# Kernel optimization log

Hardware: AMD Instinct MI355X
Metric: run time of the kernel (lower is better)

The kernel has to match this reference:

```python
import jax, jax.numpy as jnp
import numpy as np

B, T, E = 16, 1024, 1024
G, N, D = 4, 8, 128
V = 2048


def setup_inputs() -> dict:
    key = jax.random.key(0)
    k1, k2, k3, k4 = jax.random.split(key, 4)
    x_emb = jax.random.normal(k1, (B, T, E), dtype=jnp.float32)
    W_in = jax.random.normal(k2, (E, G * N * D), dtype=jnp.float32) / np.sqrt(E)
    R = jax.random.normal(k3, (G, N, D, D), dtype=jnp.float32) / np.sqrt(D)
    b = jnp.zeros((G, N, D), dtype=jnp.float32)
    W_proj = jax.random.normal(k4, (V, N * D), dtype=jnp.float32) / np.sqrt(D)
    b_proj = jnp.zeros((V,), dtype=jnp.float32)
    return {"x_emb": x_emb, "W_in": W_in, "R": R, "b": b, "W_proj": W_proj, "b_proj": b_proj}


def reference(x_emb, W_in, R, b, W_proj, b_proj):
    # Input projection for all timesteps at once: [B,T,G,N,D]
    Bx, Tx, Ex = x_emb.shape
    Wx = jnp.einsum('bte,eg->btg', x_emb, W_in).reshape(Bx, Tx, G, N, D)

    def step(carry, wx_t):
        h, c = carry  # [B,N,D] each
        # per-head matrix recurrence: R[g] @ h  -> [B,G,N,D]
        gates = wx_t + jnp.einsum('gnde,bne->bgnd', R, h) + b
        i = jax.nn.sigmoid(gates[:, 0])
        f = jax.nn.sigmoid(gates[:, 1])
        z = jnp.tanh(gates[:, 2])
        o = jax.nn.sigmoid(gates[:, 3])
        c_new = f * c + i * z
        h_new = o * jnp.tanh(c_new)
        return (h_new, c_new), h_new

    h0 = jnp.zeros((Bx, N, D), dtype=x_emb.dtype)
    c0 = jnp.zeros((Bx, N, D), dtype=x_emb.dtype)
    (hN, cN), hs = jax.lax.scan(step, (h0, c0), jnp.swapaxes(Wx, 0, 1))  # hs: [T,B,N,D]
    h_flat = jnp.swapaxes(hs, 0, 1).reshape(Bx, Tx, N * D)
    logits = jnp.einsum('btn,vn->btv', h_flat, W_proj) + b_proj
    return logits
```

## Files before the change

### kernel.cpp

```cpp
#include <hip/hip_runtime.h>
#include <hip/hip_bf16.h>

#define DEV __device__ __forceinline__

using bf16 = __hip_bfloat16;
typedef __attribute__((ext_vector_type(8))) short short8v;
typedef __attribute__((ext_vector_type(4))) float f32x4;

constexpr int Bq = 16, Tq = 1024, Eq = 1024, Gq = 4, Nq = 8, Dq = 128, Vq = 2048;
constexpr int M1 = Bq * Tq;
constexpr int N1q = Gq * Nq * Dq;
constexpr int K1 = Eq;
constexpr int K2 = Nq * Dq;
constexpr int N2 = Vq;

DEV unsigned short bfu(float x) {
  union { bf16 h; unsigned short u; } cv;
  cv.h = __float2bfloat16(x);
  return cv.u;
}

DEV float rcp_(float x) { return __builtin_amdgcn_rcpf(x); }
DEV float sigm(float x) { return rcp_(1.0f + __expf(-x)); }
DEV float tanh_(float x) { return fmaf(2.0f, rcp_(1.0f + __expf(-2.0f * x)), -1.0f); }

#define GLD16(gp, lp)                                                       \
  __builtin_amdgcn_global_load_lds(                                        \
      (const __attribute__((address_space(1))) void*)(gp),                 \
      (__attribute__((address_space(3))) void*)(lp), 16, 0, 0)

__global__ __launch_bounds__(256) void cast_f32_bf16(const float* __restrict__ s,
                                                     bf16* __restrict__ d, int n4) {
  const int i = blockIdx.x * 256 + threadIdx.x;
  if (i >= n4) return;
  const float4 v = ((const float4*)s)[i];
  ushort4 u;
  u.x = bfu(v.x); u.y = bfu(v.y); u.z = bfu(v.z); u.w = bfu(v.w);
  ((ushort4*)d)[i] = u;
}

__global__ __launch_bounds__(256) void transpose_cast_perm(const float* __restrict__ s,
                                                           bf16* __restrict__ d,
                                                           int SK, int SN) {
  __shared__ float t[32][33];
  const int n0 = blockIdx.x * 32, k0 = blockIdx.y * 32;
  const int tx = threadIdx.x & 31, ty = threadIdx.x >> 5;
#pragma unroll
  for (int i = 0; i < 32; i += 8)
    t[ty + i][tx] = s[(size_t)(k0 + ty + i) * SN + n0 + tx];
  __syncthreads();
#pragma unroll
  for (int i = 0; i < 32; i += 8) {
    const int c = n0 + ty + i;
    const int g = c >> 10, n = (c >> 7) & 7, dd = c & 127;
    const int rp = n * 512 + dd * 4 + g;
    d[(size_t)rp * SK + k0 + tx] = __float2bfloat16(t[tx][ty + i]);
  }
}

__global__ __launch_bounds__(256) void zero_flags(unsigned int* __restrict__ f) {
  f[blockIdx.x * 256 + threadIdx.x] = 0u;
}

__global__ __launch_bounds__(256) void gemm_out(const bf16* __restrict__ A,
                                                const bf16* __restrict__ Bt,
                                                float* __restrict__ C,
                                                const float* __restrict__ bp,
                                                int K, int N) {
  __shared__ bf16 As[128 * 32];
  __shared__ bf16 Bs[128 * 32];
  const int m0 = blockIdx.y * 128, n0 = blockIdx.x * 128;
  const int tid = threadIdx.x;
  const int lane = tid & 63, w = tid >> 6;
  const int wm = w >> 1, wn = w & 1;

  const int srow = lane >> 2, scol = (lane & 3) * 8;
  const int ca = w * 2;
  const bf16* Ag0 = A + (size_t)(m0 + ca * 16 + srow) * K + scol;
  const bf16* Ag1 = Ag0 + (size_t)16 * K;
  const bf16* Bg0 = Bt + (size_t)(n0 + ca * 16 + srow) * K + scol;
  const bf16* Bg1 = Bg0 + (size_t)16 * K;
  bf16* Al0 = As + ca * 512;
  bf16* Al1 = Al0 + 512;
  bf16* Bl0 = Bs + ca * 512;
  bf16* Bl1 = Bl0 + 512;

  f32x4 acc[4][4] = {};
  const int rr = lane & 15;
  const int kb = (lane >> 4) * 8;

  for (int k0 = 0; k0 < K; k0 += 32) {
    GLD16(Ag0 + k0, Al0);
    GLD16(Ag1 + k0, Al1);
    GLD16(Bg0 + k0, Bl0);
    GLD16(Bg1 + k0, Bl1);
    __syncthreads();
    short8v af[4], bfr[4];
#pragma unroll
    for (int i = 0; i < 4; ++i) {
      af[i]  = *(const short8v*)&As[(wm * 64 + i * 16 + rr) * 32 + kb];
      bfr[i] = *(const short8v*)&Bs[(wn * 64 + i * 16 + rr) * 32 + kb];
    }
#pragma unroll
    for (int i = 0; i < 4; ++i)
#pragma unroll
      for (int j = 0; j < 4; ++j)
        acc[i][j] = __builtin_amdgcn_mfma_f32_16x16x32_bf16(af[i], bfr[j], acc[i][j], 0, 0, 0);
    __syncthreads();
  }

  const int crow = (lane >> 4) * 4, ccol = lane & 15;
  float bv[4];
#pragma unroll
  for (int j = 0; j < 4; ++j) bv[j] = bp[n0 + wn * 64 + j * 16 + ccol];
#pragma unroll
  for (int i = 0; i < 4; ++i)
#pragma unroll
    for (int j = 0; j < 4; ++j) {
      const size_t base =
          (size_t)(m0 + wm * 64 + i * 16 + crow) * N + (n0 + wn * 64 + j * 16 + ccol);
#pragma unroll
      for (int jj = 0; jj < 4; ++jj)
        C[base + (size_t)jj * N] = acc[i][j][jj] + bv[j];
    }
}

__global__ __launch_bounds__(512) void fused_xw_lstm(
    const bf16* __restrict__ xb, const bf16* __restrict__ WiT,
    bf16* __restrict__ Wx, const float* __restrict__ bp,
    const float* __restrict__ R, bf16* __restrict__ h_all,
    unsigned int* flags) {
  __shared__ bf16 As[2][128 * 32];
  __shared__ bf16 Bs[2][128 * 32];
  __shared__ __align__(16) unsigned short hl[2][4][144];

  const int bid = blockIdx.x;
  const int tid = threadIdx.x;

  if (bid < 224) {
    const int lane = tid & 63;
    const int w8 = tid >> 6;
    const int ts = w8 >> 2;
    const int w = w8 & 3;
    const int wm = w >> 1, wn = w & 1;
    const int srow = lane >> 2, scol = (lane & 3) * 8;
    const int rr = lane & 15, kb = (lane >> 4) * 8;
    const int crow = (lane >> 4) * 4, ccol = lane & 15;
    bf16* Al0 = &As[ts][w * 1024];
    bf16* Al1 = Al0 + 512;
    bf16* Bl0 = &Bs[ts][w * 1024];
    bf16* Bl1 = Bl0 + 512;

    for (int pi = bid; pi < 2048; pi += 224) {
      const int tix = pi * 2 + ts;
      const int s = tix >> 9;
      const int rem = tix & 511;
      const int bn = rem >> 2, q = rem & 3;
      const int b = bn >> 3, n = bn & 7;
      const int m0 = (b * 8 + s) * 128;
      const int n0 = (n * 4 + q) * 128;

      const bf16* Ag0 = xb + (size_t)(m0 + w * 32 + srow) * 1024 + scol;
      const bf16* Ag1 = Ag0 + (size_t)16 * 1024;
      const bf16* Bg0 = WiT + (size_t)(n0 + w * 32 + srow) * 1024 + scol;
      const bf16* Bg1 = Bg0 + (size_t)16 * 1024;

      f32x4 acc[4][4] = {};
      for (int k0 = 0; k0 < 1024; k0 += 32) {
        GLD16(Ag0 + k0, Al0);
        GLD16(Ag1 + k0, Al1);
        GLD16(Bg0 + k0, Bl0);
        GLD16(Bg1 + k0, Bl1);
        __syncthreads();
        short8v af[4], bfr[4];
#pragma unroll
        for (int i = 0; i < 4; ++i) {
          af[i]  = *(const short8v*)&As[ts][(wm * 64 + i * 16 + rr) * 32 + kb];
          bfr[i] = *(const short8v*)&Bs[ts][(wn * 64 + i * 16 + rr) * 32 + kb];
        }
#pragma unroll
        for (int i = 0; i < 4; ++i)
#pragma unroll
          for (int j = 0; j < 4; ++j)
            acc[i][j] = __builtin_amdgcn_mfma_f32_16x16x32_bf16(af[i], bfr[j], acc[i][j], 0, 0, 0);
        __syncthreads();
      }

      {
        bf16* C = Wx;
#pragma unroll
        for (int i = 0; i < 4; ++i)
#pragma unroll
          for (int j = 0; j < 4; ++j) {
            const int pc = n0 + wn * 64 + j * 16 + ccol;
            const int nn = pc >> 9, gd = pc & 511;
            const int g = gd & 3, dd = gd >> 2;
            const float bvj = bp[(g * 8 + nn) * 128 + dd];
#pragma unroll
            for (int jj = 0; jj < 4; ++jj) {
              const int row = m0 + wm * 64 + i * 16 + crow + jj;
              const int bb = row >> 10, t = row & 1023;
              const size_t idx = (((size_t)(bb * 8 + nn) << 10) + t) * 512 + gd;
              C[idx] = __float2bfloat16(acc[i][j][jj] + bvj);
            }
          }
      }
      __syncthreads();
      if (tid == 0) {
        __threadfence();
#pragma unroll
        for (int k = 0; k < 2; ++k) {
          const int tx2 = pi * 2 + k;
          const int s2 = tx2 >> 9, bn2 = (tx2 & 511) >> 2;
          __hip_atomic_fetch_add(&flags[bn2 * 8 + s2], 1u,
                                 __ATOMIC_RELEASE, __HIP_MEMORY_SCOPE_AGENT);
        }
      }
    }
  } else {
    const int cid = bid - 224;
    const int n = cid & 7, bq = cid >> 3;
    const int w = tid >> 6, lane = tid & 63;
    const int lg = lane >> 4, lc = lane & 15;
    const int bloc = lc & 3;
    const int ci = lc >> 2;
    const int dsite = 16 * w + 4 * ci + lg;

    short8v Af[4][4];
#pragma unroll
    for (int tau = 0; tau < 4; ++tau) {
      const int gd = 64 * w + 16 * tau + lc;
      const int g = gd & 3, d = gd >> 2;
      const float* rbase = R + ((size_t)(g * 8 + n) * 128 + d) * 128;
#pragma unroll
      for (int kf = 0; kf < 4; ++kf) {
        const float* rp = rbase + 32 * kf + 8 * lg;
        const float4 r0 = *(const float4*)rp;
        const float4 r1 = *(const float4*)(rp + 4);
        short8v bv;
        bv[0] = (short)bfu(r0.x); bv[1] = (short)bfu(r0.y);
        bv[2] = (short)bfu(r0.z); bv[3] = (short)bfu(r0.w);
        bv[4] = (short)bfu(r1.x); bv[5] = (short)bfu(r1.y);
        bv[6] = (short)bfu(r1.z); bv[7] = (short)bfu(r1.w);
        Af[tau][kf] = bv;
      }
    }

    for (int i = tid; i < 4 * 144; i += 512) (&hl[0][0][0])[i] = 0;
    __syncthreads();

    const bf16* wxb =
        Wx + ((size_t)((bq * 4 + bloc) * 8 + n) << 10) * 512 + dsite * 4;
    bf16* hout = h_all + ((size_t)(bq * 4 + bloc) << 20) + n * 128 + dsite;

    float c = 0.f;

    for (int s = 0; s < 8; ++s) {
      if (tid == 0) {
#pragma unroll
        for (int j = 0; j < 4; ++j) {
          const int fidx = ((bq * 4 + j) * 8 + n) * 8 + s;
          while (__hip_atomic_load(&flags[fidx], __ATOMIC_RELAXED,
                                   __HIP_MEMORY_SCOPE_AGENT) < 4u)
            __builtin_amdgcn_s_sleep(2);
        }
        __threadfence();
      }
      __syncthreads();

      ushort4 wxr[4];
#pragma unroll
      for (int u = 0; u < 4; ++u)
        wxr[u] = *(const ushort4*)(wxb + (size_t)(s * 128 + u) * 512);

      const int tend = s * 128 + 128;
      for (int t0 = s * 128; t0 < tend; t0 += 4) {
#pragma unroll
        for (int u = 0; u < 4; ++u) {
          const int t = t0 + u;
          const unsigned short* hb = &hl[t & 1][0][0];
          short8v Bf[4];
#pragma unroll
          for (int kf = 0; kf < 4; ++kf)
            Bf[kf] = *(const short8v*)(hb + bloc * 144 + kf * 32 + lg * 8);

          const ushort4 wxc = wxr[u];

          f32x4 acc[4];
#pragma unroll
          for (int tau = 0; tau < 4; ++tau) {
            acc[tau][0] = 0.f; acc[tau][1] = 0.f;
            acc[tau][2] = 0.f; acc[tau][3] = 0.f;
          }
#pragma unroll
          for (int kf = 0; kf < 4; ++kf)
#pragma unroll
            for (int tau = 0; tau < 4; ++tau)
              acc[tau] = __builtin_amdgcn_mfma_f32_16x16x32_bf16(
                  Af[tau][kf], Bf[kf], acc[tau], 0, 0, 0);

          {
            const int tp = (t + 4 < tend) ? (t + 4) : (tend - 1);
            wxr[u] = *(const ushort4*)(wxb + (size_t)tp * 512);
          }

          float pre0 = (ci & 2) ? ((ci & 1) ? acc[3][0] : acc[2][0])
                                : ((ci & 1) ? acc[1][0] : acc[0][0]);
          float pre1 = (ci & 2) ? ((ci & 1) ? acc[3][1] : acc[2][1])
                                : ((ci & 1) ? acc[1][1] : acc[0][1]);
          float pre2 = (ci & 2) ? ((ci & 1) ? acc[3][2] : acc[2][2])
                                : ((ci & 1) ? acc[1][2] : acc[0][2]);
          float pre3 = (ci & 2) ? ((ci & 1) ? acc[3][3] : acc[2][3])
                                : ((ci & 1) ? acc[1][3] : acc[0][3]);
          pre0 += __uint_as_float((unsigned)wxc.x << 16);
          pre1 += __uint_as_float((unsigned)wxc.y << 16);
          pre2 += __uint_as_float((unsigned)wxc.z << 16);
          pre3 += __uint_as_float((unsigned)wxc.w << 16);

          const float i_ = sigm(pre0);
          const float f_ = sigm(pre1);
          const float z_ = tanh_(pre2);
          const float o_ = sigm(pre3);
          c = f_ * c + i_ * z_;
          const float h = o_ * tanh_(c);
          const bf16 h16 = __float2bfloat16(h);

          hl[(t + 1) & 1][bloc][dsite] = ((const unsigned short*)&h16)[0];
          hout[(size_t)t << 10] = h16;

          __builtin_amdgcn_sched_barrier(0);
          asm volatile("s_waitcnt lgkmcnt(0)" ::: "memory");
          __builtin_amdgcn_sched_barrier(0);
          __builtin_amdgcn_s_barrier();
          __builtin_amdgcn_sched_barrier(0);
        }
      }
    }
  }
}

extern "C" void kernel_launch(void* const* d_in, const int* in_sizes, int n_in,
                              void* d_out, int out_size, void* d_ws, size_t ws_size,
                              hipStream_t stream) {
  const float* x_emb = (const float*)d_in[0];
  const float* W_in  = (const float*)d_in[1];
  const float* R     = (const float*)d_in[2];
  const float* bias  = (const float*)d_in[3];
  const float* W_prj = (const float*)d_in[4];
  const float* b_prj = (const float*)d_in[5];

  char* ws = (char*)d_ws;
  bf16* xb  = (bf16*)ws;
  bf16* WiT = (bf16*)(ws + (size_t)M1 * K1 * 2);
  bf16* Wpb = WiT + (size_t)N1q * K1;
  bf16* H   = Wpb + (size_t)N2 * K2;
  unsigned int* flags = (unsigned int*)(ws + ((size_t)76 << 20));
  bf16* Wx = (bf16*)d_out;

  cast_f32_bf16<<<(M1 * K1 / 4 + 255) / 256, 256, 0, stream>>>(x_emb, xb, M1 * K1 / 4);
  transpose_cast_perm<<<dim3(N1q / 32, K1 / 32), 256, 0, stream>>>(W_in, WiT, K1, N1q);
  cast_f32_bf16<<<(N2 * K2 / 4 + 255) / 256, 256, 0, stream>>>(W_prj, Wpb, N2 * K2 / 4);
  zero_flags<<<4, 256, 0, stream>>>(flags);

  fused_xw_lstm<<<dim3(256), dim3(512), 0, stream>>>(xb, WiT, Wx, bias, R, H, flags);

  gemm_out<<<dim3(N2 / 128, M1 / 128), 256, 0, stream>>>(
      H, Wpb, (float*)d_out, b_prj, K2, N2);
}
```

Baseline: 805.7 us.

## Share A tile across wave groups and pipeline GEMM loads with 4-stage LDS ring

The input-projection GEMM blocks now load the A (x) tile once and share it between the two wave groups, each of which computes a different 128-column N tile. Previously each group loaded its own A and B tiles. The K loop becomes a 4-buffer ring that prefetches two chunks ahead, using explicit vmcnt waits and raw s_barrier instead of two __syncthreads per iteration. The aim is to halve A traffic and hide global-to-LDS latency, at the cost of more LDS for the recurrent blocks sharing the kernel and tighter hand-written waitcnt logic. The flag update is also merged into a single atomic add of 2.

```diff
diff --git a/kernel.cpp b/kernel.cpp
--- a/kernel.cpp
+++ b/kernel.cpp
@@ -28,6 +28,13 @@
   __builtin_amdgcn_global_load_lds(                                        \
       (const __attribute__((address_space(1))) void*)(gp),                 \
       (__attribute__((address_space(3))) void*)(lp), 16, 0, 0)
+
+#define SBAR0() __builtin_amdgcn_sched_barrier(0)
+#define RAWBAR()                                                            \
+  do { SBAR0(); __builtin_amdgcn_s_barrier(); SBAR0(); } while (0)
+#define VMW6() asm volatile("s_waitcnt vmcnt(6)" ::: "memory")
+#define VMW3() asm volatile("s_waitcnt vmcnt(3)" ::: "memory")
+#define VMW0() asm volatile("s_waitcnt vmcnt(0)" ::: "memory")
 
 __global__ __launch_bounds__(256) void cast_f32_bf16(const float* __restrict__ s,
                                                      bf16* __restrict__ d, int n4) {
@@ -130,8 +137,8 @@
     bf16* __restrict__ Wx, const float* __restrict__ bp,
     const float* __restrict__ R, bf16* __restrict__ h_all,
     unsigned int* flags) {
-  __shared__ bf16 As[2][128 * 32];
-  __shared__ bf16 Bs[2][128 * 32];
+  __shared__ bf16 Ab[4][128 * 32];
+  __shared__ bf16 Bb[4][2][128 * 32];
   __shared__ __align__(16) unsigned short hl[2][4][144];
 
   const int bid = blockIdx.x;
@@ -141,58 +148,76 @@
     const int lane = tid & 63;
     const int w8 = tid >> 6;
     const int ts = w8 >> 2;
-    const int w = w8 & 3;
-    const int wm = w >> 1, wn = w & 1;
-    const int srow = lane >> 2, scol = (lane & 3) * 8;
+    const int w4 = w8 & 3;
+    const int wm = w4 >> 1, wn = w4 & 1;
     const int rr = lane & 15, kb = (lane >> 4) * 8;
     const int crow = (lane >> 4) * 4, ccol = lane & 15;
-    bf16* Al0 = &As[ts][w * 1024];
-    bf16* Al1 = Al0 + 512;
-    bf16* Bl0 = &Bs[ts][w * 1024];
-    bf16* Bl1 = Bl0 + 512;
+    const int frow = 16 * w8 + (lane >> 2);
+    const int fcol = (lane & 3) * 8;
+    bf16* const Adst = &Ab[0][16 * w8 * 32];
+    bf16* const B0dst = &Bb[0][0][16 * w8 * 32];
+    bf16* const B1dst = &Bb[0][1][16 * w8 * 32];
 
     for (int pi = bid; pi < 2048; pi += 224) {
-      const int tix = pi * 2 + ts;
-      const int s = tix >> 9;
-      const int rem = tix & 511;
-      const int bn = rem >> 2, q = rem & 3;
+      const int tix0 = pi * 2;
+      const int s = tix0 >> 9;
+      const int rem = tix0 & 511;
+      const int bn = rem >> 2, q0 = rem & 3;
       const int b = bn >> 3, n = bn & 7;
       const int m0 = (b * 8 + s) * 128;
-      const int n0 = (n * 4 + q) * 128;
-
-      const bf16* Ag0 = xb + (size_t)(m0 + w * 32 + srow) * 1024 + scol;
-      const bf16* Ag1 = Ag0 + (size_t)16 * 1024;
-      const bf16* Bg0 = WiT + (size_t)(n0 + w * 32 + srow) * 1024 + scol;
-      const bf16* Bg1 = Bg0 + (size_t)16 * 1024;
+      const int n0base = (n * 4 + q0) * 128;
+
+      const bf16* Asrc = xb + (size_t)(m0 + frow) * 1024 + fcol;
+      const bf16* B0src = WiT + (size_t)(n0base + frow) * 1024 + fcol;
+      const bf16* B1src = B0src + (size_t)128 * 1024;
+
+#define FILLCHUNK(BUF, KC)                                                   \
+  do {                                                                       \
+    const size_t go_ = (size_t)(KC) * 32;                                    \
+    GLD16(Asrc + go_, Adst + (BUF) * 4096);                                  \
+    GLD16(B0src + go_, B0dst + (BUF) * 8192);                                \
+    GLD16(B1src + go_, B1dst + (BUF) * 8192);                                \
+  } while (0)
 
       f32x4 acc[4][4] = {};
-      for (int k0 = 0; k0 < 1024; k0 += 32) {
-        GLD16(Ag0 + k0, Al0);
-        GLD16(Ag1 + k0, Al1);
-        GLD16(Bg0 + k0, Bl0);
-        GLD16(Bg1 + k0, Bl1);
-        __syncthreads();
-        short8v af[4], bfr[4];
-#pragma unroll
-        for (int i = 0; i < 4; ++i) {
-          af[i]  = *(const short8v*)&As[ts][(wm * 64 + i * 16 + rr) * 32 + kb];
-          bfr[i] = *(const short8v*)&Bs[ts][(wn * 64 + i * 16 + rr) * 32 + kb];
-        }
+
+#define COMPUTECHUNK(BUF)                                                    \
+  do {                                                                       \
+    const bf16* Ap_ = &Ab[(BUF)][0];                                         \
+    const bf16* Bp_ = &Bb[(BUF)][ts][0];                                     \
+    short8v af[4], bfr[4];                                                   \
+    _Pragma("unroll") for (int i2 = 0; i2 < 4; ++i2) {                       \
+      af[i2]  = *(const short8v*)&Ap_[(wm * 64 + i2 * 16 + rr) * 32 + kb];   \
+      bfr[i2] = *(const short8v*)&Bp_[(wn * 64 + i2 * 16 + rr) * 32 + kb];   \
+    }                                                                        \
+    _Pragma("unroll") for (int i2 = 0; i2 < 4; ++i2)                         \
+      _Pragma("unroll") for (int j2 = 0; j2 < 4; ++j2)                       \
+        acc[i2][j2] = __builtin_amdgcn_mfma_f32_16x16x32_bf16(               \
+            af[i2], bfr[j2], acc[i2][j2], 0, 0, 0);                          \
+  } while (0)
+
+      FILLCHUNK(0, 0);
+      FILLCHUNK(1, 1);
+      for (int i = 0; i < 30; ++i) {
+        FILLCHUNK((i + 2) & 3, i + 2);
+        VMW6();
+        RAWBAR();
+        COMPUTECHUNK(i & 3);
+      }
+      VMW3();
+      RAWBAR();
+      COMPUTECHUNK(2);
+      VMW0();
+      RAWBAR();
+      COMPUTECHUNK(3);
+
+      {
+        const int n0t = n0base + ts * 128;
 #pragma unroll
         for (int i = 0; i < 4; ++i)
 #pragma unroll
-          for (int j = 0; j < 4; ++j)
-            acc[i][j] = __builtin_amdgcn_mfma_f32_16x16x32_bf16(af[i], bfr[j], acc[i][j], 0, 0, 0);
-        __syncthreads();
-      }
-
-      {
-        bf16* C = Wx;
-#pragma unroll
-        for (int i = 0; i < 4; ++i)
-#pragma unroll
           for (int j = 0; j < 4; ++j) {
-            const int pc = n0 + wn * 64 + j * 16 + ccol;
+            const int pc = n0t + wn * 64 + j * 16 + ccol;
             const int nn = pc >> 9, gd = pc & 511;
             const int g = gd & 3, dd = gd >> 2;
             const float bvj = bp[(g * 8 + nn) * 128 + dd];
@@ -201,22 +226,19 @@
               const int row = m0 + wm * 64 + i * 16 + crow + jj;
               const int bb = row >> 10, t = row & 1023;
               const size_t idx = (((size_t)(bb * 8 + nn) << 10) + t) * 512 + gd;
-              C[idx] = __float2bfloat16(acc[i][j][jj] + bvj);
+              Wx[idx] = __float2bfloat16(acc[i][j][jj] + bvj);
             }
           }
       }
       __syncthreads();
       if (tid == 0) {
         __threadfence();
-#pragma unroll
-        for (int k = 0; k < 2; ++k) {
-          const int tx2 = pi * 2 + k;
-          const int s2 = tx2 >> 9, bn2 = (tx2 & 511) >> 2;
-          __hip_atomic_fetch_add(&flags[bn2 * 8 + s2], 1u,
-                                 __ATOMIC_RELEASE, __HIP_MEMORY_SCOPE_AGENT);
-        }
-      }
-    }
+        __hip_atomic_fetch_add(&flags[bn * 8 + s], 2u,
+                               __ATOMIC_RELEASE, __HIP_MEMORY_SCOPE_AGENT);
+      }
+    }
+#undef FILLCHUNK
+#undef COMPUTECHUNK
   } else {
     const int cid = bid - 224;
     const int n = cid & 7, bq = cid >> 3;
```

New measurement: 767.8 us. 1.05x faster.
